# Kernel optimization log

Measured on AMD Instinct MI355X. Metric: run time of the kernel, lower is better.

The kernel has to match this reference:

```python
import jax, jax.numpy as jnp
import numpy as np

HID = 256
NH = 8
HD = HID // NH
B = 4096
N = 64


def _xavier(key, shape):
    fan_in, fan_out = shape
    lim = float(np.sqrt(6.0 / (fan_in + fan_out)))
    return jax.random.uniform(key, shape, jnp.float32, -lim, lim)


def setup_inputs() -> dict:
    key = jax.random.key(0)
    ks = jax.random.split(key, 16)
    inp = {
        "h_recv": jax.random.normal(ks[0], (B, HID), jnp.float32),
        "h_send": jax.random.normal(ks[1], (B, N, HID), jnp.float32),
        "dist_matrix": jax.random.uniform(ks[2], (B, N), jnp.float32),
        "mask": jax.random.randint(ks[3], (B, N), 0, 2, jnp.int32),
        # projection weights stored as [in, out] (transposed vs torch Linear)
        "wq_w": _xavier(ks[4], (HID, HID)), "wq_b": jnp.zeros((HID,), jnp.float32),
        "wk_w": _xavier(ks[5], (HID, HID)), "wk_b": jnp.zeros((HID,), jnp.float32),
        "wv_w": _xavier(ks[6], (HID, HID)), "wv_b": jnp.zeros((HID,), jnp.float32),
        "d1_w": _xavier(ks[7], (HID, HID // 2)), "d1_b": jnp.zeros((HID // 2,), jnp.float32),
        "d2_w": _xavier(ks[8], (HID // 2, NH)), "d2_b": jnp.zeros((NH,), jnp.float32),
    }
    return inp


def reference(h_recv, h_send, dist_matrix, mask,
              wq_w, wq_b, wk_w, wk_b, wv_w, wv_b,
              d1_w, d1_b, d2_w, d2_b):
    b, n, hid = h_send.shape
    nh = d2_b.shape[0]
    hd = hid // nh
    # projections
    Q = (h_recv @ wq_w + wq_b).reshape(b, nh, hd)            # [B,H,D]
    K = (h_send @ wk_w + wk_b).reshape(b, n, nh, hd)          # [B,N,H,D]
    V = (h_send @ wv_w + wv_b).reshape(b, n, nh, hd)          # [B,N,H,D]
    # single-query scores per head
    scores = jnp.einsum('bhd,bnhd->bnh', Q, K) / (hd ** 0.5)  # [B,N,H]
    # MLP distance bias (softplus ensures positive slope)
    b1 = jax.nn.softplus(jax.nn.relu(h_recv @ d1_w + d1_b) @ d2_w + d2_b)  # [B,H]
    scores = scores - b1[:, None, :] * dist_matrix[:, :, None]
    # mask: zero entries -> -inf
    scores = jnp.where(mask[:, :, None] != 0, scores, -jnp.inf)
    attn = jax.nn.softmax(scores, axis=1)                     # softmax over neighbors
    z = jnp.einsum('bnh,bnhd->bhd', attn, V).reshape(b, hid)  # [B,hidden]
    return z, attn
```

## Files before the change

### kernel.cpp

```cpp
#include <hip/hip_runtime.h>
#include <math.h>

#define B_   4096
#define N_   64
#define HID_ 256
#define NH_  8
#define HD_  32
#define INV_SQRT_HD 0.17677669529663687f

__global__ __launch_bounds__(256, 2) void k1_proj(
    const float* __restrict__ h_recv,
    const float* __restrict__ wq_w, const float* __restrict__ wq_b,
    const float* __restrict__ wk_w, const float* __restrict__ wk_b,
    const float* __restrict__ d1_w, const float* __restrict__ d1_b,
    const float* __restrict__ d2_w, const float* __restrict__ d2_b,
    float* __restrict__ qh_ws, float* __restrict__ b1_ws, float* __restrict__ konst_ws)
{
    __shared__ __align__(16) float hr[8][256];
    __shared__ __align__(16) float Q[8][256];
    __shared__ float R1[8][128];
    const int t = threadIdx.x;
    const int brow = blockIdx.x * 8;

    {
        const float4* src = (const float4*)(h_recv + (size_t)brow * 256);
        float4* dst = (float4*)&hr[0][0];
        dst[t] = src[t];
        dst[t + 256] = src[t + 256];
    }
    __syncthreads();

    {
        const int j = t;
        float acc[8];
        const float bq = wq_b[j];
#pragma unroll
        for (int bb = 0; bb < 8; bb++) acc[bb] = bq;
        for (int c4 = 0; c4 < 64; c4++) {
            const float w0 = wq_w[(c4 * 4 + 0) * 256 + j];
            const float w1 = wq_w[(c4 * 4 + 1) * 256 + j];
            const float w2 = wq_w[(c4 * 4 + 2) * 256 + j];
            const float w3 = wq_w[(c4 * 4 + 3) * 256 + j];
#pragma unroll
            for (int bb = 0; bb < 8; bb++) {
                const float4 h = *(const float4*)&hr[bb][c4 * 4];
                acc[bb] += h.x * w0 + h.y * w1 + h.z * w2 + h.w * w3;
            }
        }
#pragma unroll
        for (int bb = 0; bb < 8; bb++) Q[bb][j] = acc[bb];
    }
    __syncthreads();

    {
        const int j = t & 127;
        const int bg = t >> 7;
        float acc[4];
        const float bd = d1_b[j];
#pragma unroll
        for (int r = 0; r < 4; r++) acc[r] = bd;
        for (int c4 = 0; c4 < 64; c4++) {
            const float w0 = d1_w[(c4 * 4 + 0) * 128 + j];
            const float w1 = d1_w[(c4 * 4 + 1) * 128 + j];
            const float w2 = d1_w[(c4 * 4 + 2) * 128 + j];
            const float w3 = d1_w[(c4 * 4 + 3) * 128 + j];
#pragma unroll
            for (int r = 0; r < 4; r++) {
                const float4 h = *(const float4*)&hr[bg * 4 + r][c4 * 4];
                acc[r] += h.x * w0 + h.y * w1 + h.z * w2 + h.w * w3;
            }
        }
#pragma unroll
        for (int r = 0; r < 4; r++) R1[bg * 4 + r][j] = fmaxf(acc[r], 0.0f);
    }
    __syncthreads();

    if (t < 64) {
        const int bb = t >> 3, h = t & 7;
        float acc = d2_b[h];
        for (int jj = 0; jj < 128; jj++) acc += R1[bb][jj] * d2_w[jj * 8 + h];
        const float sp = (acc > 20.0f) ? acc : log1pf(expf(acc));
        b1_ws[(size_t)(brow + bb) * 8 + h] = sp;
        float k = 0.0f;
        for (int d = 0; d < 32; d++) k += Q[bb][h * 32 + d] * wk_b[h * 32 + d];
        konst_ws[(size_t)(brow + bb) * 8 + h] = k * INV_SQRT_HD;
    }

    {
        const int c = t;
        for (int h = 0; h < 8; h++) {
            float acc[8] = {0, 0, 0, 0, 0, 0, 0, 0};
#pragma unroll
            for (int d4 = 0; d4 < 8; d4++) {
                const float4 w = *(const float4*)&wk_w[(size_t)c * 256 + h * 32 + d4 * 4];
#pragma unroll
                for (int bb = 0; bb < 8; bb++) {
                    const float4 q = *(const float4*)&Q[bb][h * 32 + d4 * 4];
                    acc[bb] += q.x * w.x + q.y * w.y + q.z * w.z + q.w * w.w;
                }
            }
#pragma unroll
            for (int bb = 0; bb < 8; bb++)
                qh_ws[((size_t)(brow + bb) * 8 + h) * 256 + c] = acc[bb];
        }
    }
}

template <bool ZIN>
__global__ __launch_bounds__(256, 2) void k2_attn(
    const float* __restrict__ h_send,
    const float* __restrict__ dist, const int* __restrict__ mask,
    const float* __restrict__ qh_ws, const float* __restrict__ b1_ws,
    const float* __restrict__ konst_ws,
    float* __restrict__ attn_out,
    float* __restrict__ ctx_ws,
    const float* __restrict__ wv_w, const float* __restrict__ wv_b,
    float* __restrict__ z_out)
{
    __shared__ __align__(16) float hs[64][260];
    __shared__ __align__(16) float qh[8][260];
    __shared__ float sc[64][9];
    __shared__ float dist_l[64];
    __shared__ float b1_l[8], kon_l[8];
    __shared__ int mask_l[64];

    const int t = threadIdx.x;
    const int b = blockIdx.x;
    const int w = t >> 6;
    const int l = t & 63;

    {
        const float4* src = (const float4*)(h_send + (size_t)b * 16384);
#pragma unroll
        for (int i = 0; i < 16; i++) {
            const int q = t + 256 * i;
            *(float4*)&hs[q >> 6][(q & 63) * 4] = src[q];
        }
        const float4* qsrc = (const float4*)(qh_ws + (size_t)b * 2048);
        {
            int q = t;
            *(float4*)&qh[q >> 6][(q & 63) * 4] = qsrc[q];
            q = t + 256;
            *(float4*)&qh[q >> 6][(q & 63) * 4] = qsrc[q];
        }
        if (t < 64) {
            dist_l[t] = dist[(size_t)b * 64 + t];
            mask_l[t] = mask[(size_t)b * 64 + t];
        } else if (t < 72) {
            b1_l[t - 64] = b1_ws[(size_t)b * 8 + (t - 64)];
            kon_l[t - 64] = konst_ws[(size_t)b * 8 + (t - 64)];
        }
    }
    __syncthreads();

    {
        const int n = w * 16 + (l & 15);
        const int cq = l >> 4;
        float p[8] = {0, 0, 0, 0, 0, 0, 0, 0};
#pragma unroll 4
        for (int c4 = 0; c4 < 16; c4++) {
            const int cc = cq * 64 + c4 * 4;
            const float4 hv = *(const float4*)&hs[n][cc];
#pragma unroll
            for (int h = 0; h < 8; h++) {
                const float4 qv = *(const float4*)&qh[h][cc];
                p[h] += hv.x * qv.x + hv.y * qv.y + hv.z * qv.z + hv.w * qv.w;
            }
        }
#pragma unroll
        for (int h = 0; h < 8; h++) {
            p[h] += __shfl_xor(p[h], 16, 64);
            p[h] += __shfl_xor(p[h], 32, 64);
        }
        if (cq == 0) {
            const float dv = dist_l[n];
            const int mv = mask_l[n];
#pragma unroll
            for (int h = 0; h < 8; h++) {
                const float s = p[h] * INV_SQRT_HD + kon_l[h] - b1_l[h] * dv;
                sc[n][h] = mv ? s : -1e30f;
            }
        }
    }
    __syncthreads();

    {
        const int h = 2 * w + (l >> 5);
        const int n0 = l & 31;
        const float v0 = sc[n0][h], v1 = sc[n0 + 32][h];
        float m = fmaxf(v0, v1);
#pragma unroll
        for (int s = 1; s < 32; s <<= 1) m = fmaxf(m, __shfl_xor(m, s, 64));
        const float e0 = __expf(v0 - m), e1 = __expf(v1 - m);
        float sum = e0 + e1;
#pragma unroll
        for (int s = 1; s < 32; s <<= 1) sum += __shfl_xor(sum, s, 64);
        const float inv = 1.0f / sum;
        sc[n0][h] = e0 * inv;
        sc[n0 + 32][h] = e1 * inv;
    }
    __syncthreads();

    {
        attn_out[(size_t)b * 512 + t] = sc[t >> 3][t & 7];
        attn_out[(size_t)b * 512 + t + 256] = sc[(t + 256) >> 3][t & 7];
    }

    {
        const int h = t >> 5;
        const int l32 = t & 31;
        float4 a0 = make_float4(0.f, 0.f, 0.f, 0.f);
        float4 a1 = make_float4(0.f, 0.f, 0.f, 0.f);
        for (int n = 0; n < 64; n++) {
            const float at = sc[n][h];
            const float4 h0 = *(const float4*)&hs[n][4 * l32];
            const float4 h1 = *(const float4*)&hs[n][4 * l32 + 128];
            a0.x += at * h0.x; a0.y += at * h0.y; a0.z += at * h0.z; a0.w += at * h0.w;
            a1.x += at * h1.x; a1.y += at * h1.y; a1.z += at * h1.z; a1.w += at * h1.w;
        }
        if (!ZIN) {
            float4* co = (float4*)(ctx_ws + ((size_t)b * 8 + h) * 256);
            co[l32] = a0;
            co[l32 + 32] = a1;
        } else {
            *(float4*)&qh[h][4 * l32] = a0;
            *(float4*)&qh[h][4 * l32 + 128] = a1;
        }
    }

    if (ZIN) {
        __syncthreads();
        const int j = t;
        const int h = j >> 5;
        float acc = wv_b[j];
        for (int c4 = 0; c4 < 64; c4++) {
            const float4 cv = *(const float4*)&qh[h][c4 * 4];
            acc += cv.x * wv_w[(c4 * 4 + 0) * 256 + j] + cv.y * wv_w[(c4 * 4 + 1) * 256 + j]
                 + cv.z * wv_w[(c4 * 4 + 2) * 256 + j] + cv.w * wv_w[(c4 * 4 + 3) * 256 + j];
        }
        z_out[(size_t)b * 256 + j] = acc;
    }
}

__global__ __launch_bounds__(256, 2) void k3_z(
    const float* __restrict__ ctx_ws, const float* __restrict__ wv_w,
    const float* __restrict__ wv_b, float* __restrict__ z_out)
{
    const int t = threadIdx.x;
    const int tj = t & 63, tb = t >> 6;
    const int j0 = tj * 4;
    const int h = tj >> 3;
    const int b0 = blockIdx.x * 8 + tb * 2;
    const int b1r = b0 + 1;

    const float4 bias = *(const float4*)&wv_b[j0];
    float4 a0 = bias, a1 = bias;
    const float* c0p = ctx_ws + ((size_t)b0 * 8 + h) * 256;
    const float* c1p = ctx_ws + ((size_t)b1r * 8 + h) * 256;
    for (int c4 = 0; c4 < 64; c4++) {
        const float4 x0 = *(const float4*)&c0p[c4 * 4];
        const float4 x1 = *(const float4*)&c1p[c4 * 4];
        const float4 w0 = *(const float4*)&wv_w[(c4 * 4 + 0) * 256 + j0];
        const float4 w1 = *(const float4*)&wv_w[(c4 * 4 + 1) * 256 + j0];
        const float4 w2 = *(const float4*)&wv_w[(c4 * 4 + 2) * 256 + j0];
        const float4 w3 = *(const float4*)&wv_w[(c4 * 4 + 3) * 256 + j0];
        a0.x += x0.x * w0.x + x0.y * w1.x + x0.z * w2.x + x0.w * w3.x;
        a0.y += x0.x * w0.y + x0.y * w1.y + x0.z * w2.y + x0.w * w3.y;
        a0.z += x0.x * w0.z + x0.y * w1.z + x0.z * w2.z + x0.w * w3.z;
        a0.w += x0.x * w0.w + x0.y * w1.w + x0.z * w2.w + x0.w * w3.w;
        a1.x += x1.x * w0.x + x1.y * w1.x + x1.z * w2.x + x1.w * w3.x;
        a1.y += x1.x * w0.y + x1.y * w1.y + x1.z * w2.y + x1.w * w3.y;
        a1.z += x1.x * w0.z + x1.y * w1.z + x1.z * w2.z + x1.w * w3.z;
        a1.w += x1.x * w0.w + x1.y * w1.w + x1.z * w2.w + x1.w * w3.w;
    }
    *(float4*)&z_out[(size_t)b0 * 256 + j0] = a0;
    *(float4*)&z_out[(size_t)b1r * 256 + j0] = a1;
}

extern "C" void kernel_launch(void* const* d_in, const int* in_sizes, int n_in,
                              void* d_out, int out_size, void* d_ws, size_t ws_size,
                              hipStream_t stream)
{
    const float* h_recv = (const float*)d_in[0];
    const float* h_send = (const float*)d_in[1];
    const float* dist   = (const float*)d_in[2];
    const int*   mask   = (const int*)d_in[3];
    const float* wq_w = (const float*)d_in[4];
    const float* wq_b = (const float*)d_in[5];
    const float* wk_w = (const float*)d_in[6];
    const float* wk_b = (const float*)d_in[7];
    const float* wv_w = (const float*)d_in[8];
    const float* wv_b = (const float*)d_in[9];
    const float* d1_w = (const float*)d_in[10];
    const float* d1_b = (const float*)d_in[11];
    const float* d2_w = (const float*)d_in[12];
    const float* d2_b = (const float*)d_in[13];

    float* z_out = (float*)d_out;
    float* attn_out = (float*)d_out + (size_t)B_ * HID_;

    float* ws = (float*)d_ws;
    const size_t QH = (size_t)B_ * 8 * 256;
    const size_t need_primary = (QH * 2 + (size_t)B_ * 8 * 2) * sizeof(float);
    const bool primary = ws_size >= need_primary;

    float* qh_ws = ws;
    size_t off = QH;
    float* ctx_ws = nullptr;
    if (primary) { ctx_ws = ws + off; off += QH; }
    float* b1_ws = ws + off; off += (size_t)B_ * 8;
    float* konst_ws = ws + off;

    k1_proj<<<512, 256, 0, stream>>>(h_recv, wq_w, wq_b, wk_w, wk_b,
                                     d1_w, d1_b, d2_w, d2_b,
                                     qh_ws, b1_ws, konst_ws);
    if (primary) {
        k2_attn<false><<<B_, 256, 0, stream>>>(h_send, dist, mask, qh_ws, b1_ws, konst_ws,
                                               attn_out, ctx_ws, wv_w, wv_b, z_out);
        k3_z<<<512, 256, 0, stream>>>(ctx_ws, wv_w, wv_b, z_out);
    } else {
        k2_attn<true><<<B_, 256, 0, stream>>>(h_send, dist, mask, qh_ws, b1_ws, konst_ws,
                                              attn_out, nullptr, wv_w, wv_b, z_out);
    }
}
```

Baseline: 510.1 us.

## Fuse V-projection into attention kernel and load h_send directly into LDS

Drops the separate k3_z kernel and the ctx workspace round trip. Every attention block now computes its per-head context in LDS and applies wv_w in place. The h_send tile is loaded with global_load_lds (global-to-LDS without staging in registers), and the score and Q buffers get new LDS layouts for float4 broadcast reads. The cost is that each block streams the full wv_w matrix, which adds a lot of L2 traffic compared with the batched k3 kernel.

```diff
diff --git a/kernel.cpp b/kernel.cpp
--- a/kernel.cpp
+++ b/kernel.cpp
@@ -7,6 +7,9 @@
 #define NH_  8
 #define HD_  32
 #define INV_SQRT_HD 0.17677669529663687f
+
+typedef const float __attribute__((address_space(1)))* gbl_fp;
+typedef float __attribute__((address_space(3)))* lds_fp;
 
 __global__ __launch_bounds__(256, 2) void k1_proj(
     const float* __restrict__ h_recv,
@@ -106,20 +109,18 @@
     }
 }
 
-template <bool ZIN>
 __global__ __launch_bounds__(256, 2) void k2_attn(
     const float* __restrict__ h_send,
     const float* __restrict__ dist, const int* __restrict__ mask,
     const float* __restrict__ qh_ws, const float* __restrict__ b1_ws,
     const float* __restrict__ konst_ws,
-    float* __restrict__ attn_out,
-    float* __restrict__ ctx_ws,
     const float* __restrict__ wv_w, const float* __restrict__ wv_b,
-    float* __restrict__ z_out)
+    float* __restrict__ z_out,
+    float* __restrict__ attn_out)
 {
     __shared__ __align__(16) float hs[64][260];
-    __shared__ __align__(16) float qh[8][260];
-    __shared__ float sc[64][9];
+    __shared__ __align__(16) float qh2[8][4][68];
+    __shared__ __align__(16) float sc4[64][8];
     __shared__ float dist_l[64];
     __shared__ float b1_l[8], kon_l[8];
     __shared__ int mask_l[64];
@@ -130,18 +131,24 @@
     const int l = t & 63;
 
     {
-        const float4* src = (const float4*)(h_send + (size_t)b * 16384);
+        const float* src = h_send + (size_t)b * 16384;
 #pragma unroll
         for (int i = 0; i < 16; i++) {
-            const int q = t + 256 * i;
-            *(float4*)&hs[q >> 6][(q & 63) * 4] = src[q];
-        }
+            const int row = i * 4 + w;
+            __builtin_amdgcn_global_load_lds((gbl_fp)(src + row * 256 + l * 4),
+                                             (lds_fp)&hs[row][0], 16, 0, 0);
+        }
+    }
+    {
         const float4* qsrc = (const float4*)(qh_ws + (size_t)b * 2048);
-        {
-            int q = t;
-            *(float4*)&qh[q >> 6][(q & 63) * 4] = qsrc[q];
-            q = t + 256;
-            *(float4*)&qh[q >> 6][(q & 63) * 4] = qsrc[q];
+#pragma unroll
+        for (int k = 0; k < 2; k++) {
+            const int e = t + k * 256;
+            const float4 v = qsrc[e];
+            const int h = e >> 6;
+            const int qq = (e & 63) >> 4;
+            const int pos = (e & 15) * 4;
+            *(float4*)&qh2[h][qq][pos] = v;
         }
         if (t < 64) {
             dist_l[t] = dist[(size_t)b * 64 + t];
@@ -159,11 +166,10 @@
         float p[8] = {0, 0, 0, 0, 0, 0, 0, 0};
 #pragma unroll 4
         for (int c4 = 0; c4 < 16; c4++) {
-            const int cc = cq * 64 + c4 * 4;
-            const float4 hv = *(const float4*)&hs[n][cc];
+            const float4 hv = *(const float4*)&hs[n][cq * 64 + c4 * 4];
 #pragma unroll
             for (int h = 0; h < 8; h++) {
-                const float4 qv = *(const float4*)&qh[h][cc];
+                const float4 qv = *(const float4*)&qh2[h][cq][c4 * 4];
                 p[h] += hv.x * qv.x + hv.y * qv.y + hv.z * qv.z + hv.w * qv.w;
             }
         }
@@ -178,7 +184,7 @@
 #pragma unroll
             for (int h = 0; h < 8; h++) {
                 const float s = p[h] * INV_SQRT_HD + kon_l[h] - b1_l[h] * dv;
-                sc[n][h] = mv ? s : -1e30f;
+                sc4[n][h] = mv ? s : -1e30f;
             }
         }
     }
@@ -187,7 +193,7 @@
     {
         const int h = 2 * w + (l >> 5);
         const int n0 = l & 31;
-        const float v0 = sc[n0][h], v1 = sc[n0 + 32][h];
+        const float v0 = sc4[n0][h], v1 = sc4[n0 + 32][h];
         float m = fmaxf(v0, v1);
 #pragma unroll
         for (int s = 1; s < 32; s <<= 1) m = fmaxf(m, __shfl_xor(m, s, 64));
@@ -196,85 +202,57 @@
 #pragma unroll
         for (int s = 1; s < 32; s <<= 1) sum += __shfl_xor(sum, s, 64);
         const float inv = 1.0f / sum;
-        sc[n0][h] = e0 * inv;
-        sc[n0 + 32][h] = e1 * inv;
-    }
-    __syncthreads();
-
-    {
-        attn_out[(size_t)b * 512 + t] = sc[t >> 3][t & 7];
-        attn_out[(size_t)b * 512 + t + 256] = sc[(t + 256) >> 3][t & 7];
-    }
-
-    {
-        const int h = t >> 5;
-        const int l32 = t & 31;
-        float4 a0 = make_float4(0.f, 0.f, 0.f, 0.f);
-        float4 a1 = make_float4(0.f, 0.f, 0.f, 0.f);
-        for (int n = 0; n < 64; n++) {
-            const float at = sc[n][h];
-            const float4 h0 = *(const float4*)&hs[n][4 * l32];
-            const float4 h1 = *(const float4*)&hs[n][4 * l32 + 128];
-            a0.x += at * h0.x; a0.y += at * h0.y; a0.z += at * h0.z; a0.w += at * h0.w;
-            a1.x += at * h1.x; a1.y += at * h1.y; a1.z += at * h1.z; a1.w += at * h1.w;
-        }
-        if (!ZIN) {
-            float4* co = (float4*)(ctx_ws + ((size_t)b * 8 + h) * 256);
-            co[l32] = a0;
-            co[l32 + 32] = a1;
-        } else {
-            *(float4*)&qh[h][4 * l32] = a0;
-            *(float4*)&qh[h][4 * l32 + 128] = a1;
-        }
-    }
-
-    if (ZIN) {
-        __syncthreads();
+        sc4[n0][h] = e0 * inv;
+        sc4[n0 + 32][h] = e1 * inv;
+    }
+    __syncthreads();
+
+    {
+        const float* sl = &sc4[0][0];
+        attn_out[(size_t)b * 512 + t] = sl[t];
+        attn_out[(size_t)b * 512 + t + 256] = sl[t + 256];
+    }
+
+    float acc[8] = {0, 0, 0, 0, 0, 0, 0, 0};
+    {
+        const int c = t;
+        for (int n = 0; n < 64; n += 2) {
+            const float4 a0 = *(const float4*)&sc4[n][0];
+            const float4 a1 = *(const float4*)&sc4[n][4];
+            const float4 c0 = *(const float4*)&sc4[n + 1][0];
+            const float4 c1 = *(const float4*)&sc4[n + 1][4];
+            const float h0 = hs[n][c];
+            const float h1 = hs[n + 1][c];
+            acc[0] += a0.x * h0 + c0.x * h1;
+            acc[1] += a0.y * h0 + c0.y * h1;
+            acc[2] += a0.z * h0 + c0.z * h1;
+            acc[3] += a0.w * h0 + c0.w * h1;
+            acc[4] += a1.x * h0 + c1.x * h1;
+            acc[5] += a1.y * h0 + c1.y * h1;
+            acc[6] += a1.z * h0 + c1.z * h1;
+            acc[7] += a1.w * h0 + c1.w * h1;
+        }
+    }
+    {
+        float* cl = &qh2[0][0][0];
+#pragma unroll
+        for (int h = 0; h < 8; h++) cl[h * 272 + t] = acc[h];
+    }
+    __syncthreads();
+
+    {
         const int j = t;
-        const int h = j >> 5;
-        float acc = wv_b[j];
+        const float* cl = &qh2[0][0][0] + (j >> 5) * 272;
+        float accz = wv_b[j];
         for (int c4 = 0; c4 < 64; c4++) {
-            const float4 cv = *(const float4*)&qh[h][c4 * 4];
-            acc += cv.x * wv_w[(c4 * 4 + 0) * 256 + j] + cv.y * wv_w[(c4 * 4 + 1) * 256 + j]
-                 + cv.z * wv_w[(c4 * 4 + 2) * 256 + j] + cv.w * wv_w[(c4 * 4 + 3) * 256 + j];
-        }
-        z_out[(size_t)b * 256 + j] = acc;
-    }
-}
-
-__global__ __launch_bounds__(256, 2) void k3_z(
-    const float* __restrict__ ctx_ws, const float* __restrict__ wv_w,
-    const float* __restrict__ wv_b, float* __restrict__ z_out)
-{
-    const int t = threadIdx.x;
-    const int tj = t & 63, tb = t >> 6;
-    const int j0 = tj * 4;
-    const int h = tj >> 3;
-    const int b0 = blockIdx.x * 8 + tb * 2;
-    const int b1r = b0 + 1;
-
-    const float4 bias = *(const float4*)&wv_b[j0];
-    float4 a0 = bias, a1 = bias;
-    const float* c0p = ctx_ws + ((size_t)b0 * 8 + h) * 256;
-    const float* c1p = ctx_ws + ((size_t)b1r * 8 + h) * 256;
-    for (int c4 = 0; c4 < 64; c4++) {
-        const float4 x0 = *(const float4*)&c0p[c4 * 4];
-        const float4 x1 = *(const float4*)&c1p[c4 * 4];
-        const float4 w0 = *(const float4*)&wv_w[(c4 * 4 + 0) * 256 + j0];
-        const float4 w1 = *(const float4*)&wv_w[(c4 * 4 + 1) * 256 + j0];
-        const float4 w2 = *(const float4*)&wv_w[(c4 * 4 + 2) * 256 + j0];
-        const float4 w3 = *(const float4*)&wv_w[(c4 * 4 + 3) * 256 + j0];
-        a0.x += x0.x * w0.x + x0.y * w1.x + x0.z * w2.x + x0.w * w3.x;
-        a0.y += x0.x * w0.y + x0.y * w1.y + x0.z * w2.y + x0.w * w3.y;
-        a0.z += x0.x * w0.z + x0.y * w1.z + x0.z * w2.z + x0.w * w3.z;
-        a0.w += x0.x * w0.w + x0.y * w1.w + x0.z * w2.w + x0.w * w3.w;
-        a1.x += x1.x * w0.x + x1.y * w1.x + x1.z * w2.x + x1.w * w3.x;
-        a1.y += x1.x * w0.y + x1.y * w1.y + x1.z * w2.y + x1.w * w3.y;
-        a1.z += x1.x * w0.z + x1.y * w1.z + x1.z * w2.z + x1.w * w3.z;
-        a1.w += x1.x * w0.w + x1.y * w1.w + x1.z * w2.w + x1.w * w3.w;
-    }
-    *(float4*)&z_out[(size_t)b0 * 256 + j0] = a0;
-    *(float4*)&z_out[(size_t)b1r * 256 + j0] = a1;
+            const float4 cv = *(const float4*)&cl[c4 * 4];
+            accz += cv.x * wv_w[(c4 * 4 + 0) * 256 + j]
+                  + cv.y * wv_w[(c4 * 4 + 1) * 256 + j]
+                  + cv.z * wv_w[(c4 * 4 + 2) * 256 + j]
+                  + cv.w * wv_w[(c4 * 4 + 3) * 256 + j];
+        }
+        z_out[(size_t)b * 256 + j] = accz;
+    }
 }
 
 extern "C" void kernel_launch(void* const* d_in, const int* in_sizes, int n_in,
@@ -301,25 +279,13 @@
 
     float* ws = (float*)d_ws;
     const size_t QH = (size_t)B_ * 8 * 256;
-    const size_t need_primary = (QH * 2 + (size_t)B_ * 8 * 2) * sizeof(float);
-    const bool primary = ws_size >= need_primary;
-
     float* qh_ws = ws;
-    size_t off = QH;
-    float* ctx_ws = nullptr;
-    if (primary) { ctx_ws = ws + off; off += QH; }
-    float* b1_ws = ws + off; off += (size_t)B_ * 8;
-    float* konst_ws = ws + off;
+    float* b1_ws = ws + QH;
+    float* konst_ws = b1_ws + (size_t)B_ * 8;
 
     k1_proj<<<512, 256, 0, stream>>>(h_recv, wq_w, wq_b, wk_w, wk_b,
                                      d1_w, d1_b, d2_w, d2_b,
                                      qh_ws, b1_ws, konst_ws);
-    if (primary) {
-        k2_attn<false><<<B_, 256, 0, stream>>>(h_send, dist, mask, qh_ws, b1_ws, konst_ws,
-                                               attn_out, ctx_ws, wv_w, wv_b, z_out);
-        k3_z<<<512, 256, 0, stream>>>(ctx_ws, wv_w, wv_b, z_out);
-    } else {
-        k2_attn<true><<<B_, 256, 0, stream>>>(h_send, dist, mask, qh_ws, b1_ws, konst_ws,
-                                              attn_out, nullptr, wv_w, wv_b, z_out);
-    }
+    k2_attn<<<B_, 256, 0, stream>>>(h_send, dist, mask, qh_ws, b1_ws, konst_ws,
+                                    wv_w, wv_b, z_out, attn_out);
 }
```

After: 514.8 us. Within noise of the previous version (+0.9%).
